# Performance work log

Hardware: AMD Instinct MI355X
Metric: run time of the kernel (lower is better)

## Reference

```python
import jax, jax.numpy as jnp
import numpy as np

B, S, D = 2, 2048, 1024
INNER = 2 * D          # Mamba expand=2
STATE = 16             # Mamba state_dim
E, TOPK = 8, 2         # MoE experts / experts_per_token
CAP, TEMP = 0.5, 1.0   # MoD capacity / temperature
EPS = 1e-5
LB_W = 0.01


def setup_inputs() -> dict:
    key = jax.random.key(0)
    ks = jax.random.split(key, 12)
    g = lambda k, shp: jax.random.normal(k, shp, jnp.float32) * 0.02
    return {
        'x': jax.random.normal(ks[0], (B, S, D), jnp.float32),
        'ln1_w': jnp.ones((D,), jnp.float32), 'ln1_b': jnp.zeros((D,), jnp.float32),
        'ln2_w': jnp.ones((D,), jnp.float32), 'ln2_b': jnp.zeros((D,), jnp.float32),
        'modr_w1': g(ks[1], (D, D // 4)), 'modr_b1': jnp.zeros((D // 4,), jnp.float32),
        'modr_w2': g(ks[2], (D // 4, 1)), 'modr_b2': jnp.zeros((1,), jnp.float32),
        'm_in_w': g(ks[3], (D, 2 * INNER)),
        'm_conv_w': g(ks[4], (INNER, 4)), 'm_conv_b': jnp.zeros((INNER,), jnp.float32),
        'm_xproj_w': g(ks[5], (INNER, 2 * STATE + 1)),
        'm_out_w': g(ks[6], (INNER, D)),
        'moe_r_w': g(ks[7], (D, E)), 'moe_r_b': jnp.zeros((E,), jnp.float32),
        'moe_w1': g(ks[8], (E, D, 4 * D)), 'moe_b1': jnp.zeros((E, 4 * D), jnp.float32),
        'moe_w2': g(ks[9], (E, 4 * D, D)), 'moe_b2': jnp.zeros((E, D), jnp.float32),
    }


def _ln(t, w, b):
    mu = t.mean(-1, keepdims=True)
    var = jnp.mean((t - mu) ** 2, -1, keepdims=True)
    return (t - mu) * jax.lax.rsqrt(var + EPS) * w + b


def reference(x, ln1_w, ln1_b, ln2_w, ln2_b,
              modr_w1, modr_b1, modr_w2, modr_b2,
              m_in_w, m_conv_w, m_conv_b, m_xproj_w, m_out_w,
              moe_r_w, moe_r_b, moe_w1, moe_b1, moe_w2, moe_b2):
    B_, S_, D_ = x.shape
    k = int(S_ * CAP)
    # ---- MoD router: top-k tokens per row ----
    hr = jax.nn.relu(x @ modr_w1 + modr_b1)
    scores = (hr @ modr_w2 + modr_b2)[..., 0] / TEMP                 # [B,S]
    topk_scores, topk_idx = jax.lax.top_k(scores, k)
    w = jax.nn.softmax(topk_scores, -1)                              # [B,k], topk order
    # torch masked-assign semantics: softmax weights (topk order) land on index-sorted positions
    sorted_idx = jnp.sort(topk_idx, -1)                              # [B,k]
    sel = jnp.take_along_axis(x, sorted_idx[..., None], axis=1)      # [B,k,D]
    tok = sel.reshape(B_ * k, D_)                                    # routed tokens, 2D like x[mask]
    # ---- Mamba block on 2D input (seq_len == 1 per token) ----
    n1 = _ln(tok, ln1_w, ln1_b)
    uv = n1 @ m_in_w                                                 # [N, 2*INNER]
    u, res = uv[:, :INNER], uv[:, INNER:]
    u = u * m_conv_w[:, 3] + m_conv_b                                # depthwise conv, only tap 3 hits a len-1 seq
    sp = u @ m_xproj_w                                               # [N, 2*STATE+1]
    Bv = sp[:, STATE:2 * STATE]                                      # [N, STATE]
    Cv = sp[:, -1]                                                   # [N]
    # single selective-scan step from h0 = 0: h[d,n] = u[d]*Bv[n]; y[d] = C * sum_n h[d,n]
    y = u * (Bv.sum(-1) * Cv)[:, None]
    y = y * jax.nn.silu(res)
    attn = y @ m_out_w                                               # [N, D]
    tok = tok + attn
    n2 = _ln(tok, ln2_w, ln2_b)
    # ---- MoE (dense expert compute, gate zeros out unselected experts) ----
    logits = n2 @ moe_r_w + moe_r_b                                  # [N,E]
    rw, sel_e = jax.lax.top_k(jax.nn.softmax(logits, -1), TOPK)      # [N,TOPK]
    rw = rw / rw.sum(-1, keepdims=True)
    N = tok.shape[0]
    gate = jnp.zeros((N, E), x.dtype).at[jnp.arange(N)[:, None], sel_e].add(rw)
    h1 = jax.nn.gelu(jnp.einsum('nd,edh->enh', n2, moe_w1) + moe_b1[:, None, :], approximate=False)
    eo = jnp.einsum('enh,ehd->end', h1, moe_w2) + moe_b2[:, None, :]
    moe_out = jnp.einsum('end,ne->nd', eo, gate)
    tok = tok + moe_out
    # load-balance aux loss (unbiased variance, like torch .var())
    cnt = jax.nn.one_hot(sel_e, E, dtype=jnp.float32).sum(0)         # [TOPK,E]
    lb = jnp.var(cnt, ddof=1) / jnp.mean(cnt) * LB_W
    # ---- write routed tokens back, scaled by routing weights ----
    out = x.at[jnp.arange(B_)[:, None], sorted_idx].set(tok.reshape(B_, k, D_) * w[..., None])
    return out, lb
```

## Files before the change

kernel.cpp:

```cpp
#include <hip/hip_runtime.h>
#include <cstdint>
#include <cstddef>


typedef __bf16 bf16;
typedef bf16 bf16x4 __attribute__((ext_vector_type(4)));
typedef bf16 bf16x8 __attribute__((ext_vector_type(8)));
typedef float f32x4 __attribute__((ext_vector_type(4)));

#define DEV __device__ __forceinline__

constexpr int BB   = 2;
constexpr int S    = 2048;
constexpr int D    = 1024;
constexpr int KSEL = 1024;
constexpr int NTOK = BB * KSEL;
constexpr int INNER = 2048;
constexpr int HID  = 4096;
constexpr int NE   = 8;
constexpr float EPSF = 1e-5f;

DEV void gload_lds16(const void* g, void* l) {
  __builtin_amdgcn_global_load_lds(
      (const __attribute__((address_space(1))) void*)g,
      (__attribute__((address_space(3))) void*)l, 16, 0, 0);
}

DEV float wave_red_sum(float v) {
#pragma unroll
  for (int o = 32; o > 0; o >>= 1) v += __shfl_xor(v, o, 64);
  return v;
}

__global__ __launch_bounds__(256)
void prep_kernel(const float* __restrict__ xp, float* __restrict__ wB,
                 float* __restrict__ wC, const float* __restrict__ convw,
                 const float* __restrict__ convb, float* __restrict__ cpack,
                 int* __restrict__ ecnt, int* __restrict__ fill,
                 float* __restrict__ cnt, int* __restrict__ zeroi) {
  int bid = blockIdx.x, t = threadIdx.x;
  if (bid == 0) {
    if (t < 8) { ecnt[t] = 0; fill[t] = 0; }
    if (t < 16) cnt[t] = 0.f;
    if (t == 0) zeroi[0] = 0;
  }
  if (bid < 8) {
    int d = bid * 256 + t;
    const float* r = xp + (size_t)d * 33;
    float s = 0.f;
#pragma unroll
    for (int j = 16; j < 32; j++) s += r[j];
    wB[d] = s;
    wC[d] = r[32];
  } else {
    int i = (bid - 8) * 256 + t;
    cpack[i] = (i < INNER * 4) ? convw[i] : convb[i - INNER * 4];
  }
}

__global__ __launch_bounds__(256)
void convT_kernel(const float* __restrict__ in, bf16* __restrict__ out, int R, int C) {
  in  += (size_t)blockIdx.z * R * C;
  out += (size_t)blockIdx.z * R * C;
  __shared__ float t[32][33];
  int c0 = blockIdx.x * 32, r0 = blockIdx.y * 32;
  int tx = threadIdx.x & 31, ty = threadIdx.x >> 5;
#pragma unroll
  for (int i = 0; i < 4; i++) {
    int r = ty + i * 8;
    t[r][tx] = in[(size_t)(r0 + r) * C + c0 + tx];
  }
  __syncthreads();
#pragma unroll
  for (int i = 0; i < 4; i++) {
    int c = ty + i * 8;
    out[(size_t)(c0 + c) * R + r0 + tx] = (bf16)t[tx][c];
  }
}

__global__ __launch_bounds__(256)
void score_kernel(const float* __restrict__ x, const float* __restrict__ w1,
                  const float* __restrict__ b1, const float* __restrict__ w2,
                  const float* __restrict__ b2, float* __restrict__ scores) {
  __shared__ float As[8][8];
  __shared__ float Bsh[8][256];
  __shared__ float red[8][64];
  int tid = threadIdx.x;
  int m0 = blockIdx.x * 8;
  int tj = tid & 63, tm = tid >> 6;
  float acc[2][4] = {};
  for (int k0 = 0; k0 < 1024; k0 += 8) {
    if (tid < 64) {
      int r = tid >> 3, kk = tid & 7;
      As[kk][r] = x[(size_t)(m0 + r) * 1024 + k0 + kk];
    }
    {
      int kk = tid >> 5, j0 = (tid & 31) * 8;
      const float4* src = (const float4*)&w1[(size_t)(k0 + kk) * 256 + j0];
      float4 v0 = src[0], v1 = src[1];
      *(float4*)&Bsh[kk][j0] = v0;
      *(float4*)&Bsh[kk][j0 + 4] = v1;
    }
    __syncthreads();
#pragma unroll
    for (int k = 0; k < 8; k++) {
      float2 a = *(const float2*)&As[k][tm * 2];
      float4 bq = *(const float4*)&Bsh[k][tj * 4];
      acc[0][0] += a.x * bq.x; acc[0][1] += a.x * bq.y;
      acc[0][2] += a.x * bq.z; acc[0][3] += a.x * bq.w;
      acc[1][0] += a.y * bq.x; acc[1][1] += a.y * bq.y;
      acc[1][2] += a.y * bq.z; acc[1][3] += a.y * bq.w;
    }
    __syncthreads();
  }
  float4 b1v = *(const float4*)&b1[tj * 4];
  float4 w2v = *(const float4*)&w2[tj * 4];
  float b1a[4] = {b1v.x, b1v.y, b1v.z, b1v.w};
  float w2a[4] = {w2v.x, w2v.y, w2v.z, w2v.w};
#pragma unroll
  for (int i = 0; i < 2; i++) {
    float pacc = 0.f;
#pragma unroll
    for (int j = 0; j < 4; j++) {
      float h = fmaxf(acc[i][j] + b1a[j], 0.f);
      pacc += h * w2a[j];
    }
    red[tm * 2 + i][tj] = pacc;
  }
  __syncthreads();
  if (tid < 8) {
    float s = 0.f;
    for (int q = 0; q < 64; q++) s += red[tid][q];
    scores[m0 + tid] = s + b2[0];
  }
}

__global__ __launch_bounds__(256)
void rank_kernel(const float* __restrict__ scores, int* __restrict__ rnk) {
  int b = blockIdx.x >> 5, grp = blockIdx.x & 31;
  __shared__ float sc[2048];
  __shared__ int part[64][4];
  const float* s = scores + b * 2048;
  for (int i = threadIdx.x; i < 2048; i += 256) sc[i] = s[i];
  __syncthreads();
  int tq = threadIdx.x & 63, qr = threadIdx.x >> 6;
  int idx = grp * 64 + tq;
  float v = sc[idx];
  int c = 0;
  for (int i = qr * 512; i < qr * 512 + 512; i++) {
    float o = sc[i];
    c += (o > v) || (o == v && i < idx);
  }
  part[tq][qr] = c;
  __syncthreads();
  if (qr == 0) rnk[b * 2048 + idx] = part[tq][0] + part[tq][1] + part[tq][2] + part[tq][3];
}

__global__ __launch_bounds__(1024)
void select_scan_kernel(const float* __restrict__ scores, const int* __restrict__ rnk,
                        int* __restrict__ sidx, int* __restrict__ postok,
                        float* __restrict__ wtok) {
  int b = blockIdx.x, t = threadIdx.x;
  const float* sc = scores + b * 2048;
  const int* rk = rnk + b * 2048;
  __shared__ int ts[1024];
  __shared__ float sbr[1024];
  __shared__ float wsh[1024];
  __shared__ float reds[16];
  int r0 = rk[2 * t], r1 = rk[2 * t + 1];
  int f0 = (r0 < KSEL), f1 = (r1 < KSEL);
  if (f0) sbr[r0] = sc[2 * t];
  if (f1) sbr[r1] = sc[2 * t + 1];
  ts[t] = f0 + f1;
  __syncthreads();
  for (int off = 1; off < 1024; off <<= 1) {
    int add = (t >= off) ? ts[t - off] : 0;
    __syncthreads();
    ts[t] += add;
    __syncthreads();
  }
  int excl = ts[t] - (f0 + f1);
  if (f0) sidx[b * KSEL + excl] = 2 * t;
  if (f1) sidx[b * KSEL + excl + f0] = 2 * t + 1;
  float mx = sbr[0];
  float ev = expf(sbr[t] - mx);
  float spart = wave_red_sum(ev);
  int wv = t >> 6, ln_ = t & 63;
  if (ln_ == 0) reds[wv] = spart;
  __syncthreads();
  float tot = 0.f;
#pragma unroll
  for (int q = 0; q < 16; q++) tot += reds[q];
  wsh[t] = ev / tot;
  __syncthreads();
  if (f0) { postok[b * S + 2 * t]     = excl;      wtok[b * S + 2 * t]     = wsh[excl]; }
  if (f1) { postok[b * S + 2 * t + 1] = excl + f0; wtok[b * S + 2 * t + 1] = wsh[excl + f0]; }
}

__global__ __launch_bounds__(256)
void gather_ln1_kernel(const float* __restrict__ x, const int* __restrict__ sidx,
                       const float* __restrict__ w, const float* __restrict__ b,
                       float* __restrict__ tok, bf16* __restrict__ nb) {
  int i = blockIdx.x, t = threadIdx.x;
  int b_ = i >> 10;
  int s = sidx[i];
  const float* row = x + ((size_t)b_ * S + s) * D;
  float4 v = ((const float4*)row)[t];
  float s1 = v.x + v.y + v.z + v.w;
  float s2 = v.x * v.x + v.y * v.y + v.z * v.z + v.w * v.w;
  s1 = wave_red_sum(s1);
  s2 = wave_red_sum(s2);
  __shared__ float rs[8];
  int wv = t >> 6, ln_ = t & 63;
  if (ln_ == 0) { rs[wv] = s1; rs[4 + wv] = s2; }
  __syncthreads();
  float S1 = rs[0] + rs[1] + rs[2] + rs[3];
  float S2 = rs[4] + rs[5] + rs[6] + rs[7];
  float mu = S1 * (1.f / 1024.f);
  float var = S2 * (1.f / 1024.f) - mu * mu;
  float rstd = rsqrtf(var + EPSF);
  float4 wv4 = ((const float4*)w)[t], bv4 = ((const float4*)b)[t];
  float4 o;
  o.x = (v.x - mu) * rstd * wv4.x + bv4.x;
  o.y = (v.y - mu) * rstd * wv4.y + bv4.y;
  o.z = (v.z - mu) * rstd * wv4.z + bv4.z;
  o.w = (v.w - mu) * rstd * wv4.w + bv4.w;
  ((float4*)(tok + (size_t)i * D))[t] = v;
  bf16x4 ov = {(bf16)o.x, (bf16)o.y, (bf16)o.z, (bf16)o.w};
  *(bf16x4*)(nb + (size_t)i * D + t * 4) = ov;
}

template <int MODE>
__global__ __launch_bounds__(256)
void gemm_bt(const bf16* __restrict__ A, const bf16* __restrict__ Bt,
             int M, int N, int K,
             float* __restrict__ of, bf16* __restrict__ ob,
             const float* __restrict__ e0,
             const int* __restrict__ me_p, const int* __restrict__ poff_p,
             const int* __restrict__ hoff_p,
             const int* __restrict__ al_tok, const float* __restrict__ al_w,
             size_t bt_zstride, int e0_zstride) {
  int Me = M, base = 0, hoff = 0;
  if (MODE >= 2) {
    int z = blockIdx.z;
    Me = me_p[z];
    base = poff_p[z];
    hoff = hoff_p[z];
    Bt += (size_t)z * bt_zstride;
    e0 += (size_t)z * e0_zstride;
    if ((int)blockIdx.y * 128 >= Me) return;
  }
  __shared__ bf16 As[128 * 32];
  __shared__ bf16 Bs[128 * 32];
  const int tid = threadIdx.x, lane = tid & 63, wv = tid >> 6;
  const int m0 = blockIdx.y * 128, n0 = blockIdx.x * 128;

  const int srow = lane >> 2, sq = lane & 3;
  const int ra0 = wv * 32 + srow, ra1 = ra0 + 16;
  const bf16 *ap0, *ap1;
  if (MODE == 2) {
    int r0 = m0 + ra0, r1 = m0 + ra1;
    int t0 = (r0 < Me) ? al_tok[base + r0] : 0;
    int t1 = (r1 < Me) ? al_tok[base + r1] : 0;
    ap0 = A + (size_t)t0 * K;
    ap1 = A + (size_t)t1 * K;
  } else if (MODE == 3) {
    ap0 = A + (size_t)(hoff + m0 + ra0) * K;
    ap1 = A + (size_t)(hoff + m0 + ra1) * K;
  } else {
    ap0 = A + (size_t)(m0 + ra0) * K;
    ap1 = A + (size_t)(m0 + ra1) * K;
  }
  const bf16* bp0 = Bt + (size_t)(n0 + ra0) * K;
  const bf16* bp1 = Bt + (size_t)(n0 + ra1) * K;

  bf16* lda0 = As + ((size_t)wv * 128 + lane) * 8;
  bf16* lda1 = As + ((size_t)wv * 128 + 64 + lane) * 8;
  bf16* ldb0 = Bs + ((size_t)wv * 128 + lane) * 8;
  bf16* ldb1 = Bs + ((size_t)wv * 128 + 64 + lane) * 8;

  const int g = lane >> 4, r16 = lane & 15;
  const int wr = (wv >> 1) * 64, wc = (wv & 1) * 64;

  f32x4 acc[4][4] = {};

  for (int k0 = 0; k0 < K; k0 += 32) {
    gload_lds16(ap0 + k0 + sq * 8, lda0);
    gload_lds16(ap1 + k0 + sq * 8, lda1);
    gload_lds16(bp0 + k0 + sq * 8, ldb0);
    gload_lds16(bp1 + k0 + sq * 8, ldb1);
    __syncthreads();
    bf16x8 av[4], bv[4];
#pragma unroll
    for (int m = 0; m < 4; m++)
      av[m] = *(const bf16x8*)&As[(wr + m * 16 + r16) * 32 + g * 8];
#pragma unroll
    for (int n = 0; n < 4; n++)
      bv[n] = *(const bf16x8*)&Bs[(wc + n * 16 + r16) * 32 + g * 8];
#pragma unroll
    for (int m = 0; m < 4; m++)
#pragma unroll
      for (int n = 0; n < 4; n++)
        acc[m][n] = __builtin_amdgcn_mfma_f32_16x16x32_bf16(av[m], bv[n], acc[m][n], 0, 0, 0);
    __syncthreads();
  }

#pragma unroll
  for (int m = 0; m < 4; m++) {
#pragma unroll
    for (int n = 0; n < 4; n++) {
#pragma unroll
      for (int j = 0; j < 4; j++) {
        int lr = wr + m * 16 + g * 4 + j;
        int lc = wc + n * 16 + r16;
        float c = acc[m][n][j];
        int grow = m0 + lr, gcol = n0 + lc;
        if (MODE == 0) {
          if (gcol < INNER) {
            of[(size_t)grow * INNER + gcol] = c * e0[gcol * 4 + 3] + e0[INNER * 4 + gcol];
          } else {
            float sg = c / (1.f + expf(-c));
            ob[(size_t)grow * INNER + (gcol - INNER)] = (bf16)sg;
          }
        } else if (MODE == 1) {
          of[(size_t)grow * D + gcol] += c;
        } else if (MODE == 2) {
          if (grow < Me) {
            float z = c + e0[gcol];
            float gl = 0.5f * z * (1.f + erff(z * 0.70710678118654752f));
            ob[(size_t)(hoff + grow) * HID + gcol] = (bf16)gl;
          }
        } else {
          if (grow < Me) {
            int tk = al_tok[base + grow];
            float w_ = al_w[base + grow];
            atomicAdd(&of[(size_t)tk * D + gcol], w_ * (c + e0[gcol]));
          }
        }
      }
    }
  }
}

__global__ __launch_bounds__(256)
void gdot_y_kernel(const float* __restrict__ u, bf16* __restrict__ resb,
                   const float* __restrict__ wB, const float* __restrict__ wC) {
  int i = blockIdx.x, t = threadIdx.x;
  const float4* ur = (const float4*)(u + (size_t)i * INNER);
  float4 u0 = ur[t], u1 = ur[t + 256];
  float4 b0 = ((const float4*)wB)[t], b1v = ((const float4*)wB)[t + 256];
  float4 c0 = ((const float4*)wC)[t], c1v = ((const float4*)wC)[t + 256];
  float dB = u0.x * b0.x + u0.y * b0.y + u0.z * b0.z + u0.w * b0.w
           + u1.x * b1v.x + u1.y * b1v.y + u1.z * b1v.z + u1.w * b1v.w;
  float dC = u0.x * c0.x + u0.y * c0.y + u0.z * c0.z + u0.w * c0.w
           + u1.x * c1v.x + u1.y * c1v.y + u1.z * c1v.z + u1.w * c1v.w;
  dB = wave_red_sum(dB);
  dC = wave_red_sum(dC);
  __shared__ float rs[8];
  __shared__ float gs;
  int wv = t >> 6, ln_ = t & 63;
  if (ln_ == 0) { rs[wv] = dB; rs[4 + wv] = dC; }
  __syncthreads();
  if (t == 0) gs = (rs[0] + rs[1] + rs[2] + rs[3]) * (rs[4] + rs[5] + rs[6] + rs[7]);
  __syncthreads();
  float g = gs;
  bf16x4* rp = (bf16x4*)resb + (size_t)i * 512;
  bf16x4 s0 = rp[t], s1 = rp[t + 256];
  bf16x4 y0 = {(bf16)(u0.x * g * (float)s0[0]), (bf16)(u0.y * g * (float)s0[1]),
               (bf16)(u0.z * g * (float)s0[2]), (bf16)(u0.w * g * (float)s0[3])};
  bf16x4 y1 = {(bf16)(u1.x * g * (float)s1[0]), (bf16)(u1.y * g * (float)s1[1]),
               (bf16)(u1.z * g * (float)s1[2]), (bf16)(u1.w * g * (float)s1[3])};
  rp[t] = y0;
  rp[t + 256] = y1;
}

__global__ __launch_bounds__(256)
void ln2_route_kernel(const float* __restrict__ tok, const float* __restrict__ w,
                      const float* __restrict__ b, const float* __restrict__ rwt,
                      const float* __restrict__ rb, bf16* __restrict__ nb,
                      int* __restrict__ sel_e, float* __restrict__ rwo,
                      int* __restrict__ ecnt, float* __restrict__ cnt) {
  int n = blockIdx.x, t = threadIdx.x;
  float4 v = ((const float4*)(tok + (size_t)n * D))[t];
  float s1 = v.x + v.y + v.z + v.w;
  float s2 = v.x * v.x + v.y * v.y + v.z * v.z + v.w * v.w;
  s1 = wave_red_sum(s1);
  s2 = wave_red_sum(s2);
  __shared__ float rs[8];
  __shared__ float lp[4][8];
  __shared__ float lg[8];
  int wv = t >> 6, ln_ = t & 63;
  if (ln_ == 0) { rs[wv] = s1; rs[4 + wv] = s2; }
  __syncthreads();
  float S1 = rs[0] + rs[1] + rs[2] + rs[3];
  float S2 = rs[4] + rs[5] + rs[6] + rs[7];
  float mu = S1 * (1.f / 1024.f);
  float var = S2 * (1.f / 1024.f) - mu * mu;
  float rstd = rsqrtf(var + EPSF);
  float4 wv4 = ((const float4*)w)[t], bv4 = ((const float4*)b)[t];
  float oc[4];
  oc[0] = (v.x - mu) * rstd * wv4.x + bv4.x;
  oc[1] = (v.y - mu) * rstd * wv4.y + bv4.y;
  oc[2] = (v.z - mu) * rstd * wv4.z + bv4.z;
  oc[3] = (v.w - mu) * rstd * wv4.w + bv4.w;
  bf16x4 ov = {(bf16)oc[0], (bf16)oc[1], (bf16)oc[2], (bf16)oc[3]};
  *(bf16x4*)(nb + (size_t)n * D + t * 4) = ov;
  float part[8] = {};
  const float4* wr4 = (const float4*)(rwt + (size_t)t * 32);
#pragma unroll
  for (int c = 0; c < 4; c++) {
    float4 ra = wr4[2 * c], rbq = wr4[2 * c + 1];
    part[0] += oc[c] * ra.x;  part[1] += oc[c] * ra.y;
    part[2] += oc[c] * ra.z;  part[3] += oc[c] * ra.w;
    part[4] += oc[c] * rbq.x; part[5] += oc[c] * rbq.y;
    part[6] += oc[c] * rbq.z; part[7] += oc[c] * rbq.w;
  }
#pragma unroll
  for (int e = 0; e < 8; e++) part[e] = wave_red_sum(part[e]);
  if (ln_ == 0)
#pragma unroll
    for (int e = 0; e < 8; e++) lp[wv][e] = part[e];
  __syncthreads();
  if (t == 0) {
#pragma unroll
    for (int e = 0; e < 8; e++) lg[e] = rb[e] + lp[0][e] + lp[1][e] + lp[2][e] + lp[3][e];
    float mx = lg[0];
    for (int q = 1; q < 8; q++) mx = fmaxf(mx, lg[q]);
    float p[8];
    float sm = 0.f;
    for (int q = 0; q < 8; q++) { p[q] = expf(lg[q] - mx); sm += p[q]; }
    float inv = 1.f / sm;
    for (int q = 0; q < 8; q++) p[q] *= inv;
    int e0 = 0;
    for (int q = 1; q < 8; q++) if (p[q] > p[e0]) e0 = q;
    int e1 = (e0 == 0) ? 1 : 0;
    for (int q = 0; q < 8; q++) if (q != e0 && p[q] > p[e1]) e1 = q;
    float r0 = p[e0], r1 = p[e1], iS = 1.f / (r0 + r1);
    sel_e[n * 2] = e0;
    sel_e[n * 2 + 1] = e1;
    rwo[n * 2] = r0 * iS;
    rwo[n * 2 + 1] = r1 * iS;
    atomicAdd(&ecnt[e0], 1);
    atomicAdd(&ecnt[e1], 1);
    atomicAdd(&cnt[e0], 1.f);
    atomicAdd(&cnt[8 + e1], 1.f);
  }
}

__global__ void offs_lb_kernel(const int* __restrict__ ecnt, int* __restrict__ poff,
                               const float* __restrict__ cnt, float* __restrict__ lb_out) {
  if (threadIdx.x == 0 && blockIdx.x == 0) {
    int o = 0;
    for (int e = 0; e < NE; e++) {
      poff[e] = o;
      o += (ecnt[e] + 127) & ~127;
    }
    float mu = 0.f;
    for (int i = 0; i < 16; i++) mu += cnt[i];
    mu *= (1.f / 16.f);
    float v = 0.f;
    for (int i = 0; i < 16; i++) { float d_ = cnt[i] - mu; v += d_ * d_; }
    v *= (1.f / 15.f);
    lb_out[0] = v / mu * 0.01f;
  }
}

__global__ void scatter_assign_kernel(const int* __restrict__ sel_e, const float* __restrict__ rw,
                                      const int* __restrict__ poff, int* __restrict__ fill,
                                      int* __restrict__ al_tok, float* __restrict__ al_w) {
  int a = blockIdx.x * 256 + threadIdx.x;
  if (a < NTOK * 2) {
    int n = a >> 1;
    int e = sel_e[a];
    int pzn = atomicAdd(&fill[e], 1);
    int r = poff[e] + pzn;
    al_tok[r] = n;
    al_w[r] = rw[a];
  }
}

__global__ __launch_bounds__(256)
void outwrite_kernel(const float* __restrict__ x, const float* __restrict__ tok,
                     const int* __restrict__ rnk, const int* __restrict__ postok,
                     const float* __restrict__ wtok, float* __restrict__ out) {
  int r = blockIdx.x, t = threadIdx.x;
  int b = r >> 11;
  float4 o;
  if (rnk[r] < KSEL) {
    int pos = postok[r];
    float w = wtok[r];
    float4 v = ((const float4*)(tok + ((size_t)b * KSEL + pos) * D))[t];
    o.x = v.x * w; o.y = v.y * w; o.z = v.z * w; o.w = v.w * w;
  } else {
    o = ((const float4*)(x + (size_t)r * D))[t];
  }
  ((float4*)(out + (size_t)r * D))[t] = o;
}

extern "C" void kernel_launch(void* const* d_in, const int* in_sizes, int n_in,
                              void* d_out, int out_size, void* d_ws, size_t ws_size,
                              hipStream_t stream) {
  (void)in_sizes; (void)n_in; (void)out_size;
  const float* x      = (const float*)d_in[0];
  const float* ln1w   = (const float*)d_in[1];
  const float* ln1b   = (const float*)d_in[2];
  const float* ln2w   = (const float*)d_in[3];
  const float* ln2b   = (const float*)d_in[4];
  const float* mrw1   = (const float*)d_in[5];
  const float* mrb1   = (const float*)d_in[6];
  const float* mrw2   = (const float*)d_in[7];
  const float* mrb2   = (const float*)d_in[8];
  const float* minw   = (const float*)d_in[9];
  const float* mconvw = (const float*)d_in[10];
  const float* mconvb = (const float*)d_in[11];
  const float* mxproj = (const float*)d_in[12];
  const float* moutw  = (const float*)d_in[13];
  const float* merw   = (const float*)d_in[14];
  const float* merb   = (const float*)d_in[15];
  const float* mew1   = (const float*)d_in[16];
  const float* meb1   = (const float*)d_in[17];
  const float* mew2   = (const float*)d_in[18];
  const float* meb2   = (const float*)d_in[19];
  float* out = (float*)d_out;

  const bool big = ws_size >= (size_t)206 * 1024 * 1024;

  char* p = (char*)d_ws;
  auto take = [&](size_t bytes) {
    char* r = p;
    p += (bytes + 255) & ~(size_t)255;
    return r;
  };
  float* scores = (float*)take(4096 * 4);
  int*   rnk    = (int*)take(4096 * 4);
  int*   sidx   = (int*)take(2048 * 4);
  int*   postok = (int*)take(4096 * 4);
  float* wtok   = (float*)take(4096 * 4);
  float* wB     = (float*)take(2048 * 4);
  float* wC     = (float*)take(2048 * 4);
  int*   ecnt   = (int*)take(8 * 4);
  int*   fill   = (int*)take(8 * 4);
  int*   poff   = (int*)take(8 * 4);
  int*   zeroi  = (int*)take(8 * 4);
  float* cnt    = (float*)take(16 * 4);
  int*   sel_e  = (int*)take(NTOK * 2 * 4);
  float* rwsel  = (float*)take(NTOK * 2 * 4);
  int*   altok  = (int*)take(5120 * 4);
  float* alw    = (float*)take(5120 * 4);
  float* cpack  = (float*)take((size_t)(INNER * 4 + INNER) * 4);
  float* tok    = (float*)take((size_t)NTOK * D * 4);
  bf16*  nb     = (bf16*)take((size_t)NTOK * D * 2);
  float* u      = (float*)take((size_t)NTOK * INNER * 4);
  bf16*  resb   = (bf16*)take((size_t)NTOK * INNER * 2);
  bf16*  h1     = (bf16*)take((size_t)(big ? 5120 : 2048) * HID * 2);
  bf16*  wTA    = (bf16*)take((size_t)(big ? NE : 1) * HID * D * 2);
  bf16*  wTB    = (bf16*)take((size_t)(big ? NE : 1) * HID * D * 2);

  prep_kernel<<<48, 256, 0, stream>>>(mxproj, wB, wC, mconvw, mconvb, cpack,
                                      ecnt, fill, cnt, zeroi);

  score_kernel<<<512, 256, 0, stream>>>(x, mrw1, mrb1, mrw2, mrb2, scores);
  rank_kernel<<<64, 256, 0, stream>>>(scores, rnk);
  select_scan_kernel<<<BB, 1024, 0, stream>>>(scores, rnk, sidx, postok, wtok);

  gather_ln1_kernel<<<NTOK, 256, 0, stream>>>(x, sidx, ln1w, ln1b, tok, nb);

  convT_kernel<<<dim3(128, 32, 1), 256, 0, stream>>>(minw, wTA, D, 2 * INNER);
  gemm_bt<0><<<dim3(32, 16, 1), 256, 0, stream>>>(nb, wTA, NTOK, 2 * INNER, D,
                                                  u, resb, cpack,
                                                  nullptr, nullptr, nullptr, nullptr, nullptr,
                                                  0, 0);

  gdot_y_kernel<<<NTOK, 256, 0, stream>>>(u, resb, wB, wC);

  convT_kernel<<<dim3(32, 64, 1), 256, 0, stream>>>(moutw, wTB, INNER, D);
  gemm_bt<1><<<dim3(8, 16, 1), 256, 0, stream>>>(resb, wTB, NTOK, D, INNER,
                                                 tok, nullptr, nullptr,
                                                 nullptr, nullptr, nullptr, nullptr, nullptr,
                                                 0, 0);

  ln2_route_kernel<<<NTOK, 256, 0, stream>>>(tok, ln2w, ln2b, merw, merb,
                                             nb, sel_e, rwsel, ecnt, cnt);
  offs_lb_kernel<<<1, 64, 0, stream>>>(ecnt, poff, cnt, out + (size_t)BB * S * D);
  scatter_assign_kernel<<<16, 256, 0, stream>>>(sel_e, rwsel, poff, fill, altok, alw);

  if (big) {
    convT_kernel<<<dim3(128, 32, NE), 256, 0, stream>>>(mew1, wTA, D, HID);
    gemm_bt<2><<<dim3(32, 16, NE), 256, 0, stream>>>(nb, wTA, NTOK, HID, D,
                                                     nullptr, h1, meb1,
                                                     ecnt, poff, poff, altok, alw,
                                                     (size_t)HID * D, HID);
    convT_kernel<<<dim3(32, 128, NE), 256, 0, stream>>>(mew2, wTB, HID, D);
    gemm_bt<3><<<dim3(8, 16, NE), 256, 0, stream>>>(h1, wTB, NTOK, D, HID,
                                                    tok, nullptr, meb2,
                                                    ecnt, poff, poff, altok, alw,
                                                    (size_t)D * HID, D);
  } else {
    for (int e = 0; e < NE; e++) {
      convT_kernel<<<dim3(128, 32, 1), 256, 0, stream>>>(mew1 + (size_t)e * D * HID, wTA, D, HID);
      gemm_bt<2><<<dim3(32, 16, 1), 256, 0, stream>>>(nb, wTA, NTOK, HID, D,
                                                      nullptr, h1, meb1 + (size_t)e * HID,
                                                      ecnt + e, poff + e, zeroi, altok, alw,
                                                      0, 0);
      convT_kernel<<<dim3(32, 128, 1), 256, 0, stream>>>(mew2 + (size_t)e * HID * D, wTB, HID, D);
      gemm_bt<3><<<dim3(8, 16, 1), 256, 0, stream>>>(h1, wTB, NTOK, D, HID,
                                                     tok, nullptr, meb2 + (size_t)e * D,
                                                     ecnt + e, poff + e, zeroi, altok, alw,
                                                     0, 0);
    }
  }

  outwrite_kernel<<<BB * S, 256, 0, stream>>>(x, tok, rnk, postok, wtok, out);
}
```

Before: 943.5 us.

## Double-buffer LDS tiles in bf16 GEMM to overlap global loads with MFMA

Splits the shared-memory A/B tiles into two buffers and issues the next K-slice's global-to-LDS loads before computing on the current slice, with one vmcnt wait and barrier per iteration instead of two syncthreads. This aims to hide global load latency behind the MFMA work in every GEMM mode, including the MoE expert GEMMs that dominate runtime. It doubles LDS use per block, which can lower occupancy. The manual waitcnt/barrier ordering has to be correct for LDS reads and writes to the two buffers.

```diff
diff --git a/kernel.cpp b/kernel.cpp
--- a/kernel.cpp
+++ b/kernel.cpp
@@ -240,20 +240,20 @@
              const int* __restrict__ hoff_p,
              const int* __restrict__ al_tok, const float* __restrict__ al_w,
              size_t bt_zstride, int e0_zstride) {
+  const int bx = blockIdx.x, by = blockIdx.y, bz = blockIdx.z;
   int Me = M, base = 0, hoff = 0;
   if (MODE >= 2) {
-    int z = blockIdx.z;
-    Me = me_p[z];
-    base = poff_p[z];
-    hoff = hoff_p[z];
-    Bt += (size_t)z * bt_zstride;
-    e0 += (size_t)z * e0_zstride;
-    if ((int)blockIdx.y * 128 >= Me) return;
-  }
-  __shared__ bf16 As[128 * 32];
-  __shared__ bf16 Bs[128 * 32];
+    Me = me_p[bz];
+    base = poff_p[bz];
+    hoff = hoff_p[bz];
+    Bt += (size_t)bz * bt_zstride;
+    e0 += (size_t)bz * e0_zstride;
+    if (by * 128 >= Me) return;
+  }
+  __shared__ bf16 As[2][128 * 32];
+  __shared__ bf16 Bs[2][128 * 32];
   const int tid = threadIdx.x, lane = tid & 63, wv = tid >> 6;
-  const int m0 = blockIdx.y * 128, n0 = blockIdx.x * 128;
+  const int m0 = by * 128, n0 = bx * 128;
 
   const int srow = lane >> 2, sq = lane & 3;
   const int ra0 = wv * 32 + srow, ra1 = ra0 + 16;
@@ -274,35 +274,44 @@
   const bf16* bp0 = Bt + (size_t)(n0 + ra0) * K;
   const bf16* bp1 = Bt + (size_t)(n0 + ra1) * K;
 
-  bf16* lda0 = As + ((size_t)wv * 128 + lane) * 8;
-  bf16* lda1 = As + ((size_t)wv * 128 + 64 + lane) * 8;
-  bf16* ldb0 = Bs + ((size_t)wv * 128 + lane) * 8;
-  bf16* ldb1 = Bs + ((size_t)wv * 128 + 64 + lane) * 8;
+  const int soff0 = (wv * 128 + lane) * 8;
+  const int soff1 = (wv * 128 + 64 + lane) * 8;
+  const int koff = sq * 8;
 
   const int g = lane >> 4, r16 = lane & 15;
   const int wr = (wv >> 1) * 64, wc = (wv & 1) * 64;
 
   f32x4 acc[4][4] = {};
 
-  for (int k0 = 0; k0 < K; k0 += 32) {
-    gload_lds16(ap0 + k0 + sq * 8, lda0);
-    gload_lds16(ap1 + k0 + sq * 8, lda1);
-    gload_lds16(bp0 + k0 + sq * 8, ldb0);
-    gload_lds16(bp1 + k0 + sq * 8, ldb1);
-    __syncthreads();
+  auto stage = [&](int buf, int k0) {
+    gload_lds16(ap0 + k0 + koff, &As[buf][soff0]);
+    gload_lds16(ap1 + k0 + koff, &As[buf][soff1]);
+    gload_lds16(bp0 + k0 + koff, &Bs[buf][soff0]);
+    gload_lds16(bp1 + k0 + koff, &Bs[buf][soff1]);
+  };
+
+  const int nk = K >> 5;
+  stage(0, 0);
+  asm volatile("s_waitcnt vmcnt(0)" ::: "memory");
+  __builtin_amdgcn_s_barrier();
+
+  for (int t = 0; t < nk; t++) {
+    const int cur = t & 1;
+    if (t + 1 < nk) stage(cur ^ 1, (t + 1) * 32);
     bf16x8 av[4], bv[4];
 #pragma unroll
     for (int m = 0; m < 4; m++)
-      av[m] = *(const bf16x8*)&As[(wr + m * 16 + r16) * 32 + g * 8];
+      av[m] = *(const bf16x8*)&As[cur][(wr + m * 16 + r16) * 32 + g * 8];
 #pragma unroll
     for (int n = 0; n < 4; n++)
-      bv[n] = *(const bf16x8*)&Bs[(wc + n * 16 + r16) * 32 + g * 8];
+      bv[n] = *(const bf16x8*)&Bs[cur][(wc + n * 16 + r16) * 32 + g * 8];
 #pragma unroll
     for (int m = 0; m < 4; m++)
 #pragma unroll
       for (int n = 0; n < 4; n++)
         acc[m][n] = __builtin_amdgcn_mfma_f32_16x16x32_bf16(av[m], bv[n], acc[m][n], 0, 0, 0);
-    __syncthreads();
+    asm volatile("s_waitcnt vmcnt(0)" ::: "memory");
+    __builtin_amdgcn_s_barrier();
   }
 
 #pragma unroll
```

After: 908.5 us. 3.7% less time.
